# Kernel tuning notes

Hardware: AMD Instinct MI355X
Metric: run time of the kernel (lower is better)

## Reference

```python
import jax, jax.numpy as jnp
import numpy as np

SHAPES = ((64, 64), (32, 32), (16, 16), (8, 8))
LEVEL_STARTS = np.concatenate([[0], np.cumsum([h * w for h, w in SHAPES])]).tolist()
N_LEVELS = 4; N_HEADS = 8; N_POINTS = 4; D_MODEL = 256; HEAD_DIM = 32; D_FFN = 1024; NUM_LAYERS = 2
LEN_IN = sum(h * w for h, w in SHAPES)
BATCH = 2


def setup_inputs():
    key = jax.random.key(0)
    ks = iter(jax.random.split(key, 40))
    r = lambda shape, s=1.0: jax.random.normal(next(ks), shape, dtype=jnp.float32) * s
    L = NUM_LAYERS
    return {
        "src": r((BATCH, LEN_IN, D_MODEL)),
        "pos": r((BATCH, LEN_IN, D_MODEL), 0.5),
        "valid_ratios": jnp.ones((BATCH, N_LEVELS, 2), jnp.float32),
        "Wv": r((L, D_MODEL, D_MODEL), 0.05), "bv": jnp.zeros((L, D_MODEL), jnp.float32),
        "Woff": r((L, D_MODEL, N_HEADS * N_LEVELS * N_POINTS * 2), 0.002),
        "boff": r((L, N_HEADS * N_LEVELS * N_POINTS * 2), 0.5),
        "Wa": r((L, D_MODEL, N_HEADS * N_LEVELS * N_POINTS), 0.05),
        "ba": jnp.zeros((L, N_HEADS * N_LEVELS * N_POINTS), jnp.float32),
        "Wo": r((L, D_MODEL, D_MODEL), 0.05), "bo": jnp.zeros((L, D_MODEL), jnp.float32),
        "g1": jnp.ones((L, D_MODEL), jnp.float32), "be1": jnp.zeros((L, D_MODEL), jnp.float32),
        "Wl1": r((L, D_MODEL, D_FFN), 0.05), "bl1": jnp.zeros((L, D_FFN), jnp.float32),
        "Wl2": r((L, D_FFN, D_MODEL), 0.05), "bl2": jnp.zeros((L, D_MODEL), jnp.float32),
        "g2": jnp.ones((L, D_MODEL), jnp.float32), "be2": jnp.zeros((L, D_MODEL), jnp.float32),
    }


def layer_norm(x, g, b, eps=1e-5):
    m = jnp.mean(x, -1, keepdims=True)
    v = jnp.mean(jnp.square(x - m), -1, keepdims=True)
    return (x - m) * jax.lax.rsqrt(v + eps) * g + b


def make_reference_points(valid_ratios):
    # DeformableTransformerEncoder.get_reference_points, vectorized per level
    refs = []
    for lvl, (H, W) in enumerate(SHAPES):
        gy, gx = jnp.meshgrid(jnp.arange(H, dtype=jnp.float32) + 0.5,
                              jnp.arange(W, dtype=jnp.float32) + 0.5, indexing="ij")
        ry = gy.reshape(-1)[None] / (valid_ratios[:, lvl, 1][:, None] * H)
        rx = gx.reshape(-1)[None] / (valid_ratios[:, lvl, 0][:, None] * W)
        refs.append(jnp.stack([rx, ry], -1))  # [N, H*W, 2]
    ref = jnp.concatenate(refs, 1)  # [N, Len, 2]
    return ref[:, :, None, :] * valid_ratios[:, None]  # [N, Len, n_levels, 2]


def ms_deform_attn(query, input_flatten, reference_points, Wv, bv, Woff, boff, Wa, ba, Wo, bo):
    N, Lq, _ = query.shape
    value = (input_flatten @ Wv + bv).reshape(N, -1, N_HEADS, HEAD_DIM)
    off = (query @ Woff + boff).reshape(N, Lq, N_HEADS, N_LEVELS, N_POINTS, 2)
    aw = (query @ Wa + ba).reshape(N, Lq, N_HEADS, N_LEVELS * N_POINTS)
    aw = jax.nn.softmax(aw, -1).reshape(N, Lq, N_HEADS, N_LEVELS, N_POINTS)
    # normalizer is (W, H) per level, as in MSDeformAttn
    normalizer = jnp.array([[w, h] for h, w in SHAPES], jnp.float32)
    loc = reference_points[:, :, None, :, None, :] + off / normalizer[None, None, None, :, None, :]
    acc = jnp.zeros((N, N_HEADS, Lq, HEAD_DIM), query.dtype)
    for lvl, (H, W) in enumerate(SHAPES):
        s = LEVEL_STARTS[lvl]
        val = value[:, s:s + H * W].transpose(0, 2, 1, 3)  # [N, heads, H*W, hd]
        # grid_sample bilinear, align_corners=False, zero padding
        x = loc[:, :, :, lvl, :, 0] * W - 0.5  # [N, Lq, heads, P]
        y = loc[:, :, :, lvl, :, 1] * H - 0.5
        x0 = jnp.floor(x); y0 = jnp.floor(y)
        wx1 = x - x0; wy1 = y - y0
        ix0 = x0.astype(jnp.int32); iy0 = y0.astype(jnp.int32)

        def corner(ix, iy, w):
            valid = (ix >= 0) & (ix < W) & (iy >= 0) & (iy < H)
            idx = jnp.clip(iy, 0, H - 1) * W + jnp.clip(ix, 0, W - 1)
            idx = idx.transpose(0, 2, 1, 3).reshape(N, N_HEADS, Lq * N_POINTS)
            g = jnp.take_along_axis(val, idx[..., None], axis=2).reshape(N, N_HEADS, Lq, N_POINTS, HEAD_DIM)
            w = jnp.where(valid, w, 0.0).transpose(0, 2, 1, 3)  # [N, heads, Lq, P]
            return g * w[..., None]

        sampled = (corner(ix0, iy0, (1 - wx1) * (1 - wy1))
                   + corner(ix0 + 1, iy0, wx1 * (1 - wy1))
                   + corner(ix0, iy0 + 1, (1 - wx1) * wy1)
                   + corner(ix0 + 1, iy0 + 1, wx1 * wy1))
        acc = acc + (sampled * aw[:, :, :, lvl].transpose(0, 2, 1, 3)[..., None]).sum(3)
    out = acc.transpose(0, 2, 1, 3).reshape(N, Lq, D_MODEL)
    return out @ Wo + bo


def reference(src, pos, valid_ratios, Wv, bv, Woff, boff, Wa, ba, Wo, bo,
              g1, be1, Wl1, bl1, Wl2, bl2, g2, be2):
    ref_pts = make_reference_points(valid_ratios)
    out = src
    for l in range(NUM_LAYERS):
        q = out + pos  # with_pos_embed
        attn = ms_deform_attn(q, out, ref_pts, Wv[l], bv[l], Woff[l], boff[l],
                              Wa[l], ba[l], Wo[l], bo[l])
        out = layer_norm(out + attn, g1[l], be1[l])
        ffn = jax.nn.relu(out @ Wl1[l] + bl1[l]) @ Wl2[l] + bl2[l]
        out = layer_norm(out + ffn, g2[l], be2[l])
    return out
```

## Files before the change

### kernel.cpp

```cpp
#include <hip/hip_runtime.h>
#include <math.h>

#define LEN   5440
#define NB    2
#define MROWS (NB * LEN)
#define DM    256
#define NH    8
#define HD    32
#define NLV   4
#define NPT   4
#define DFFN  1024

typedef __attribute__((ext_vector_type(8))) short bf16x8;
typedef __attribute__((ext_vector_type(4))) short bf16x4;
typedef __attribute__((ext_vector_type(4))) float f32x4;

#define MFMA16 __builtin_amdgcn_mfma_f32_16x16x32_bf16

__device__ __forceinline__ short f2bf(float f) {
    union { float f; unsigned u; } cv; cv.f = f;
    unsigned r = cv.u + 0x7fffu + ((cv.u >> 16) & 1u);
    return (short)(r >> 16);
}
__device__ __forceinline__ float bf2f(short s) {
    union { unsigned u; float f; } cv;
    cv.u = ((unsigned)(unsigned short)s) << 16;
    return cv.f;
}

__device__ __forceinline__ void gload16(const short* g, short* l) {
    __builtin_amdgcn_global_load_lds(
        (__attribute__((address_space(1))) void*)g,
        (__attribute__((address_space(3))) void*)l, 16, 0, 0);
}

template <int N> __device__ __forceinline__ void vmwait();
template <> __device__ __forceinline__ void vmwait<0>() { asm volatile("s_waitcnt vmcnt(0)" ::: "memory"); }
template <> __device__ __forceinline__ void vmwait<8>() { asm volatile("s_waitcnt vmcnt(8)" ::: "memory"); }
template <> __device__ __forceinline__ void vmwait<9>() { asm volatile("s_waitcnt vmcnt(9)" ::: "memory"); }


__global__ __launch_bounds__(256) void prep_all(
    const float* __restrict__ Wv,  const float* __restrict__ Woff,
    const float* __restrict__ Wa,  const float* __restrict__ Wo,
    const float* __restrict__ Wl1, const float* __restrict__ Wl2,
    short* __restrict__ out,
    const float4* __restrict__ s4, const float4* __restrict__ p4,
    bf16x4* __restrict__ curb, bf16x4* __restrict__ qb)
{
    __shared__ short T[32][33];
    if (blockIdx.x >= 1472) {
        const int i = (blockIdx.x - 1472) * 256 + threadIdx.x;
        float4 s = s4[i], p = p4[i];
        bf16x4 c, q;
        c[0] = f2bf(s.x); c[1] = f2bf(s.y); c[2] = f2bf(s.z); c[3] = f2bf(s.w);
        q[0] = f2bf(s.x + p.x); q[1] = f2bf(s.y + p.y);
        q[2] = f2bf(s.z + p.z); q[3] = f2bf(s.w + p.w);
        curb[i] = c; qb[i] = q;
        return;
    }
    int bx = blockIdx.x;
    int l  = bx / 736;
    int t  = bx % 736;
    const float* src; int K, N; long doff;
    if      (t < 64)  { src = Wv;   K = 256;  N = 256;  doff = 0;      }
    else if (t < 128) { src = Woff; K = 256;  N = 256;  doff = 65536;  t -= 64;  }
    else if (t < 160) { src = Wa;   K = 256;  N = 128;  doff = 131072; t -= 128; }
    else if (t < 224) { src = Wo;   K = 256;  N = 256;  doff = 163840; t -= 160; }
    else if (t < 480) { src = Wl1;  K = 256;  N = 1024; doff = 229376; t -= 224; }
    else              { src = Wl2;  K = 1024; N = 256;  doff = 491520; t -= 480; }
    src += (long)l * K * N;
    short* dst = out + (long)l * 753664 + doff;

    const int ntx = N / 32;
    const int n0 = (t % ntx) * 32, k0 = (t / ntx) * 32;

    const int tid = threadIdx.x;
    {
        const int n = tid & 31, kq = tid >> 5;
        #pragma unroll
        for (int i = 0; i < 4; ++i) {
            int k = kq * 4 + i;
            T[n][k] = f2bf(src[(long)(k0 + k) * N + n0 + n]);
        }
    }
    __syncthreads();
    {
        const int k = tid & 31, nq = tid >> 5;
        #pragma unroll
        for (int i = 0; i < 4; ++i) {
            int n = nq * 4 + i;
            dst[(long)(n0 + n) * K + k0 + k] = T[n][k];
        }
    }
}

template <int RELU, int OMODE, int K>
__device__ __forceinline__ void gemm_core128_v3(
    short* As, short* Bs,
    const short* __restrict__ A, const short* __restrict__ Wt,
    const float* __restrict__ bias, float* __restrict__ Cf,
    short* __restrict__ Cb, int ldc, int m0, int wrow0, int ccol0)
{
    constexpr int NT = K / 64;
    static_assert(NT >= 4 && (NT & 1) == 0, "NT even >= 4");
    const int t    = threadIdx.x;
    const int wave = t >> 6, lane = t & 63;
    const int wm   = (wave & 1) * 64;
    const int wn   = (wave >> 1) * 64;
    const int lm   = lane & 15;
    const int chkg = lane >> 4;

    const short* aS[4]; const short* bS[4];
    int ldst[4];
    #pragma unroll
    for (int j = 0; j < 4; ++j) {
        const int row = wave * 32 + j * 8 + (lane >> 3);
        const int sc  = (lane & 7) ^ (row & 7);
        aS[j] = A  + (long)(m0 + row) * K + sc * 8;
        bS[j] = Wt + (long)(wrow0 + row) * K + sc * 8;
        ldst[j] = wave * 2048 + j * 512;
    }

    int offA[4], offB[4];
    #pragma unroll
    for (int s = 0; s < 4; ++s) {
        const int r = wm + s * 16 + lm;
        offA[s] = r * 64 + ((chkg ^ (r & 7)) * 8);
    }
    #pragma unroll
    for (int u = 0; u < 4; ++u) {
        const int r = wn + u * 16 + lm;
        offB[u] = r * 64 + ((chkg ^ (r & 7)) * 8);
    }

    f32x4 acc[4][4] = {};

#define STG3(BUF, KT) do {                                            \
        const int _ko = (KT) * 64;                                    \
        _Pragma("unroll")                                             \
        for (int j = 0; j < 4; ++j)                                   \
            gload16(aS[j] + _ko, As + (BUF) * 8192 + ldst[j]);        \
        _Pragma("unroll")                                             \
        for (int j = 0; j < 4; ++j)                                   \
            gload16(bS[j] + _ko, Bs + (BUF) * 8192 + ldst[j]);        \
    } while (0)

#define GB3(T, BUF, WN, DOSTAGE) do {                                 \
        vmwait<WN>();                                                 \
        __builtin_amdgcn_s_barrier();                                 \
        bf16x8 a0[4], a1[4], b0[4], b1[4];                            \
        _Pragma("unroll")                                             \
        for (int s = 0; s < 4; ++s) {                                 \
            a0[s] = *(const bf16x8*)(As + (BUF) * 8192 + offA[s]);    \
            a1[s] = *(const bf16x8*)(As + (BUF) * 8192 + (offA[s] ^ 32)); \
        }                                                             \
        _Pragma("unroll")                                             \
        for (int u = 0; u < 4; ++u) {                                 \
            b0[u] = *(const bf16x8*)(Bs + (BUF) * 8192 + offB[u]);    \
            b1[u] = *(const bf16x8*)(Bs + (BUF) * 8192 + (offB[u] ^ 32)); \
        }                                                             \
        asm volatile("s_waitcnt lgkmcnt(0)" ::: "memory");            \
        __builtin_amdgcn_s_barrier();                                 \
        __builtin_amdgcn_sched_barrier(0);                            \
        if (DOSTAGE) STG3(BUF, (T) + 2);                              \
        _Pragma("unroll")                                             \
        for (int s = 0; s < 4; ++s)                                   \
            _Pragma("unroll")                                         \
            for (int u = 0; u < 4; ++u) {                             \
                acc[s][u] = MFMA16(a0[s], b0[u], acc[s][u], 0, 0, 0); \
                acc[s][u] = MFMA16(a1[s], b1[u], acc[s][u], 0, 0, 0); \
            }                                                         \
    } while (0)

    STG3(0, 0);
    STG3(1, 1);
    for (int tt = 0; tt < NT - 2; tt += 2) {
        GB3(tt,     0, 8, true);
        GB3(tt + 1, 1, 8, true);
    }
    GB3(NT - 2, 0, 8, false);
    GB3(NT - 1, 1, 0, false);
#undef GB3
#undef STG3

    const int col = lane & 15;
    const int rq  = (lane >> 4) * 4;
    #pragma unroll
    for (int s = 0; s < 4; ++s) {
        #pragma unroll
        for (int u = 0; u < 4; ++u) {
            const int gn = ccol0 + wn + u * 16 + col;
            const float bb = bias[gn];
            #pragma unroll
            for (int r = 0; r < 4; ++r) {
                const int gm = m0 + wm + s * 16 + rq + r;
                float v = acc[s][u][r] + bb;
                if (RELU) v = fmaxf(v, 0.f);
                if (OMODE == 0) {
                    Cf[(long)gm * ldc + gn] = v;
                } else if (OMODE == 1) {
                    Cb[(long)gm * ldc + gn] = f2bf(v);
                } else {
                    const int n   = gm / LEN;
                    const int pix = gm - n * LEN;
                    const int h   = gn >> 5, d = gn & 31;
                    Cb[((long)(n * NH + h) * LEN + pix) * 32 + d] = f2bf(v);
                }
            }
        }
    }
}

template <int RELU, int OMODE, int K>
__global__ __launch_bounds__(256) void gemm128v3(
    const short* __restrict__ A, const short* __restrict__ Wt,
    const float* __restrict__ bias, float* Cf, short* Cb, int ldc)
{
    __shared__ __align__(16) short As[2 * 128 * 64];
    __shared__ __align__(16) short Bs[2 * 128 * 64];
    gemm_core128_v3<RELU, OMODE, K>(As, Bs, A, Wt, bias, Cf, Cb, ldc,
                                    blockIdx.y * 128, blockIdx.x * 128,
                                    blockIdx.x * 128);
}

__global__ __launch_bounds__(256) void gemm_qkv128(
    const short* __restrict__ curb, const short* __restrict__ qb,
    const short* __restrict__ Wt, const float* __restrict__ bv,
    const float* __restrict__ boff, const float* __restrict__ ba,
    short* __restrict__ Vb, float* __restrict__ OFF, float* __restrict__ AW)
{
    __shared__ __align__(16) short As[2 * 128 * 64];
    __shared__ __align__(16) short Bs[2 * 128 * 64];
    const int n0 = blockIdx.x * 128;
    if (n0 < 256) {
        gemm_core128_v3<0, 2, 256>(As, Bs, curb, Wt, bv, (float*)nullptr, Vb,
                                   256, blockIdx.y * 128, n0, n0);
    } else if (n0 < 512) {
        gemm_core128_v3<0, 0, 256>(As, Bs, qb, Wt, boff, OFF, (short*)nullptr,
                                   256, blockIdx.y * 128, n0, n0 - 256);
    } else {
        gemm_core128_v3<0, 0, 256>(As, Bs, qb, Wt, ba, AW, (short*)nullptr,
                                   128, blockIdx.y * 128, n0, n0 - 512);
    }
}

template <int K>
__global__ __launch_bounds__(256) void gemm_ln(
    const short* __restrict__ A, const short* __restrict__ Wt,
    const float* __restrict__ bias, const short* __restrict__ residb,
    const float* __restrict__ g, const float* __restrict__ be,
    short* __restrict__ outb, short* __restrict__ outq,
    float* __restrict__ outf, const float* __restrict__ pos)
{
    constexpr int NT = K / 64;
    static_assert(NT >= 4 && (NT & 1) == 0, "NT even >= 4");
    __shared__ __align__(16) short As[2 * 32 * 64];
    __shared__ __align__(16) short Bs[2 * 256 * 64];
    __shared__ float red[2][32][2];

    const int t    = threadIdx.x;
    const int wave = t >> 6, lane = t & 63;
    const int wm   = (wave & 1) * 16;
    const int wn   = (wave >> 1) * 128;
    const int lm   = lane & 15;
    const int chkg = lane >> 4;
    const int rq   = chkg * 4;
    const int m0   = blockIdx.x * 32;

    short rr[8][4];
    #pragma unroll
    for (int u = 0; u < 8; ++u)
        #pragma unroll
        for (int r = 0; r < 4; ++r)
            rr[u][r] = residb[(long)(m0 + wm + rq + r) * DM + wn + u * 16 + lm];
    asm volatile("" ::: "memory");

    const int arow = t >> 3;
    const short* aSp = A + (long)(m0 + arow) * K + (((t & 7) ^ (arow & 7)) * 8);
    const int aDst = wave * 512;
    const short* bSp[8]; int bDst[8];
    #pragma unroll
    for (int j = 0; j < 8; ++j) {
        const int row = wave * 64 + j * 8 + (lane >> 3);
        const int sc  = (lane & 7) ^ (row & 7);
        bSp[j] = Wt + (long)row * K + sc * 8;
        bDst[j] = wave * 4096 + j * 512;
    }

    const int offA = (wm + lm) * 64 + ((chkg ^ ((wm + lm) & 7)) * 8);
    int offB[8];
    #pragma unroll
    for (int u = 0; u < 8; ++u) {
        const int r = wn + u * 16 + lm;
        offB[u] = r * 64 + ((chkg ^ (r & 7)) * 8);
    }

    f32x4 acc[8] = {};

#define STGL(BUF, KT) do {                                            \
        const int _ko = (KT) * 64;                                    \
        gload16(aSp + _ko, As + (BUF) * 2048 + aDst);                 \
        _Pragma("unroll")                                             \
        for (int j = 0; j < 8; ++j)                                   \
            gload16(bSp[j] + _ko, Bs + (BUF) * 16384 + bDst[j]);      \
    } while (0)

#define GBLN(T, BUF, WN, DOSTAGE) do {                                \
        vmwait<WN>();                                                 \
        __builtin_amdgcn_s_barrier();                                 \
        bf16x8 af0 = *(const bf16x8*)(As + (BUF) * 2048 + offA);      \
        bf16x8 af1 = *(const bf16x8*)(As + (BUF) * 2048 + (offA ^ 32)); \
        bf16x8 b0[8], b1[8];                                          \
        _Pragma("unroll")                                             \
        for (int u = 0; u < 8; ++u) {                                 \
            b0[u] = *(const bf16x8*)(Bs + (BUF) * 16384 + offB[u]);   \
            b1[u] = *(const bf16x8*)(Bs + (BUF) * 16384 + (offB[u] ^ 32)); \
        }                                                             \
        asm volatile("s_waitcnt lgkmcnt(0)" ::: "memory");            \
        __builtin_amdgcn_s_barrier();                                 \
        __builtin_amdgcn_sched_barrier(0);                            \
        if (DOSTAGE) STGL(BUF, (T) + 2);                              \
        _Pragma("unroll")                                             \
        for (int u = 0; u < 8; ++u) {                                 \
            acc[u] = MFMA16(af0, b0[u], acc[u], 0, 0, 0);             \
            acc[u] = MFMA16(af1, b1[u], acc[u], 0, 0, 0);             \
        }                                                             \
    } while (0)

    STGL(0, 0);
    STGL(1, 1);
    for (int tt = 0; tt < NT - 2; tt += 2) {
        GBLN(tt,     0, 9, true);
        GBLN(tt + 1, 1, 9, true);
    }
    GBLN(NT - 2, 0, 9, false);
    GBLN(NT - 1, 1, 0, false);
#undef GBLN
#undef STGL

    #pragma unroll
    for (int u = 0; u < 8; ++u) {
        const int gn = wn + u * 16 + lm;
        const float bb = bias[gn];
        #pragma unroll
        for (int r = 0; r < 4; ++r)
            acc[u][r] += bb + bf2f(rr[u][r]);
    }

    float rs[4], r2[4];
    #pragma unroll
    for (int r = 0; r < 4; ++r) {
        float s = 0.f, s2 = 0.f;
        #pragma unroll
        for (int u = 0; u < 8; ++u) { const float v = acc[u][r]; s += v; s2 += v * v; }
        rs[r] = s; r2[r] = s2;
    }
    #pragma unroll
    for (int o = 1; o < 16; o <<= 1)
        #pragma unroll
        for (int r = 0; r < 4; ++r) {
            rs[r] += __shfl_xor(rs[r], o, 64);
            r2[r] += __shfl_xor(r2[r], o, 64);
        }
    if (lm == 0) {
        #pragma unroll
        for (int r = 0; r < 4; ++r) {
            red[wave >> 1][wm + rq + r][0] = rs[r];
            red[wave >> 1][wm + rq + r][1] = r2[r];
        }
    }
    __syncthreads();
    #pragma unroll
    for (int r = 0; r < 4; ++r) {
        const int row = wm + rq + r;
        const float ts = red[0][row][0] + red[1][row][0];
        const float t2 = red[0][row][1] + red[1][row][1];
        const float mean = ts * (1.f / DM);
        const float var  = t2 * (1.f / DM) - mean * mean;
        rs[r] = mean;
        r2[r] = rsqrtf(var + 1e-5f);
    }
    #pragma unroll
    for (int u = 0; u < 8; ++u) {
        const int gn = wn + u * 16 + lm;
        const float gg = g[gn], bbe = be[gn];
        #pragma unroll
        for (int r = 0; r < 4; ++r) {
            const long gm = m0 + wm + rq + r;
            const float o = (acc[u][r] - rs[r]) * r2[r] * gg + bbe;
            if (outb) outb[gm * DM + gn] = f2bf(o);
            if (outq) outq[gm * DM + gn] = f2bf(o + pos[gm * DM + gn]);
            if (outf) outf[gm * DM + gn] = o;
        }
    }
}

template <int KLEN, int KSTR>
__global__ __launch_bounds__(256) void ln2_part_k(
    const short* __restrict__ A0, const short* __restrict__ Wt0,
    float* __restrict__ PART)
{
    constexpr int NT = KLEN / 64;
    static_assert(NT >= 4 && (NT & 1) == 0, "NT even >= 4");
    __shared__ __align__(16) short As[2 * 32 * 64];
    __shared__ __align__(16) short Bs[2 * 256 * 64];

    const int kk = blockIdx.x;
    const int m0 = blockIdx.y * 32;
    const short* A  = A0  + kk * KLEN;
    const short* Wt = Wt0 + kk * KLEN;
    float* Pout = PART + (long)kk * MROWS * DM;

    const int t    = threadIdx.x;
    const int wave = t >> 6, lane = t & 63;
    const int wm   = (wave & 1) * 16;
    const int wn   = (wave >> 1) * 128;
    const int lm   = lane & 15;
    const int chkg = lane >> 4;
    const int rq   = chkg * 4;

    const int arow = t >> 3;
    const short* aSp = A + (long)(m0 + arow) * KSTR + (((t & 7) ^ (arow & 7)) * 8);
    const int aDst = wave * 512;
    const short* bSp[8]; int bDst[8];
    #pragma unroll
    for (int j = 0; j < 8; ++j) {
        const int row = wave * 64 + j * 8 + (lane >> 3);
        const int sc  = (lane & 7) ^ (row & 7);
        bSp[j] = Wt + (long)row * KSTR + sc * 8;
        bDst[j] = wave * 4096 + j * 512;
    }

    const int offA = (wm + lm) * 64 + ((chkg ^ ((wm + lm) & 7)) * 8);
    int offB[8];
    #pragma unroll
    for (int u = 0; u < 8; ++u) {
        const int r = wn + u * 16 + lm;
        offB[u] = r * 64 + ((chkg ^ (r & 7)) * 8);
    }

    f32x4 acc[8] = {};

#define STGP(BUF, KT) do {                                            \
        const int _ko = (KT) * 64;                                    \
        gload16(aSp + _ko, As + (BUF) * 2048 + aDst);                 \
        _Pragma("unroll")                                             \
        for (int j = 0; j < 8; ++j)                                   \
            gload16(bSp[j] + _ko, Bs + (BUF) * 16384 + bDst[j]);      \
    } while (0)

#define GBP(T, BUF, WN, DOSTAGE) do {                                 \
        vmwait<WN>();                                                 \
        __builtin_amdgcn_s_barrier();                                 \
        bf16x8 af0 = *(const bf16x8*)(As + (BUF) * 2048 + offA);      \
        bf16x8 af1 = *(const bf16x8*)(As + (BUF) * 2048 + (offA ^ 32)); \
        bf16x8 b0[8], b1[8];                                          \
        _Pragma("unroll")                                             \
        for (int u = 0; u < 8; ++u) {                                 \
            b0[u] = *(const bf16x8*)(Bs + (BUF) * 16384 + offB[u]);   \
            b1[u] = *(const bf16x8*)(Bs + (BUF) * 16384 + (offB[u] ^ 32)); \
        }                                                             \
        asm volatile("s_waitcnt lgkmcnt(0)" ::: "memory");            \
        __builtin_amdgcn_s_barrier();                                 \
        __builtin_amdgcn_sched_barrier(0);                            \
        if (DOSTAGE) STGP(BUF, (T) + 2);                              \
        _Pragma("unroll")                                             \
        for (int u = 0; u < 8; ++u) {                                 \
            acc[u] = MFMA16(af0, b0[u], acc[u], 0, 0, 0);             \
            acc[u] = MFMA16(af1, b1[u], acc[u], 0, 0, 0);             \
        }                                                             \
    } while (0)

    STGP(0, 0);
    STGP(1, 1);
    for (int tt = 0; tt < NT - 2; tt += 2) {
        GBP(tt,     0, 9, true);
        GBP(tt + 1, 1, 9, true);
    }
    GBP(NT - 2, 0, 9, false);
    GBP(NT - 1, 1, 0, false);
#undef GBP
#undef STGP

    #pragma unroll
    for (int u = 0; u < 8; ++u) {
        const int gn = wn + u * 16 + lm;
        #pragma unroll
        for (int r = 0; r < 4; ++r)
            Pout[(long)(m0 + wm + rq + r) * DM + gn] = acc[u][r];
    }
}

__global__ __launch_bounds__(256) void ln2_fin_k(
    const float* __restrict__ PART, const short* __restrict__ residb,
    const float* __restrict__ bl2, const float* __restrict__ g,
    const float* __restrict__ be, short* __restrict__ outb,
    short* __restrict__ outq, float* __restrict__ outf,
    const float* __restrict__ pos)
{
    const int wave = threadIdx.x >> 6, lane = threadIdx.x & 63;
    const int c0 = lane * 4;
    const f32x4 bb = *(const f32x4*)(bl2 + c0);
    const f32x4 gg = *(const f32x4*)(g + c0);
    const f32x4 ee = *(const f32x4*)(be + c0);
    #pragma unroll 1
    for (int r = 0; r < 8; ++r) {
        const long row = (long)blockIdx.x * 32 + wave * 8 + r;
        const f32x4 p0 = *(const f32x4*)(PART + row * DM + c0);
        const f32x4 p1 = *(const f32x4*)(PART + (long)MROWS * DM + row * DM + c0);
        const bf16x4 rr = *(const bf16x4*)(residb + row * DM + c0);
        float v[4]; float s = 0.f, s2 = 0.f;
        #pragma unroll
        for (int j = 0; j < 4; ++j) {
            v[j] = p0[j] + p1[j] + bb[j] + bf2f(rr[j]);
            s += v[j]; s2 += v[j] * v[j];
        }
        #pragma unroll
        for (int o = 1; o < 64; o <<= 1) {
            s  += __shfl_xor(s,  o, 64);
            s2 += __shfl_xor(s2, o, 64);
        }
        const float mean = s * (1.f / DM);
        const float var  = s2 * (1.f / DM) - mean * mean;
        const float rstd = rsqrtf(var + 1e-5f);
        float o4[4];
        #pragma unroll
        for (int j = 0; j < 4; ++j)
            o4[j] = (v[j] - mean) * rstd * gg[j] + ee[j];
        if (outb) {
            bf16x4 ob;
            #pragma unroll
            for (int j = 0; j < 4; ++j) ob[j] = f2bf(o4[j]);
            *(bf16x4*)(outb + row * DM + c0) = ob;
        }
        if (outq) {
            const f32x4 pp = *(const f32x4*)(pos + row * DM + c0);
            bf16x4 oq;
            #pragma unroll
            for (int j = 0; j < 4; ++j) oq[j] = f2bf(o4[j] + pp[j]);
            *(bf16x4*)(outq + row * DM + c0) = oq;
        }
        if (outf) {
            f32x4 of;
            #pragma unroll
            for (int j = 0; j < 4; ++j) of[j] = o4[j];
            *(f32x4*)(outf + row * DM + c0) = of;
        }
    }
}

__global__ __launch_bounds__(256) void deform_attn_v3(
    const short* __restrict__ Vb,
    const float* __restrict__ OFF,
    const float* __restrict__ AW,
    const float* __restrict__ vr,
    bf16x4* __restrict__ ATTb)
{
    const int starts[5] = {0, 4096, 5120, 5376, 5440};
    const int dims[4]   = {64, 32, 16, 8};

    const int wave = threadIdx.x >> 6;
    const int lane = threadIdx.x & 63;
    const int h    = lane >> 3;
    const int d4   = lane & 7;

    const int gq = blockIdx.x * 4 + wave;
    const int n  = gq / LEN;
    const int q  = gq % LEN;

    int lq = 3;
    if (q < 4096) lq = 0; else if (q < 5120) lq = 1; else if (q < 5376) lq = 2;
    const int r  = q - starts[lq];
    const int Wq = dims[lq];
    const int gy = r / Wq, gx = r % Wq;
    const float vrxq = vr[(n * NLV + lq) * 2 + 0];
    const float vryq = vr[(n * NLV + lq) * 2 + 1];
    const float rx = (gx + 0.5f) / (vrxq * Wq);
    const float ry = (gy + 0.5f) / (vryq * Wq);

    const long row = (long)n * LEN + q;

    const float* awp = AW + row * 128 + h * 16;
    float a[16];
    float mx = -1e30f;
    #pragma unroll
    for (int i = 0; i < 16; ++i) { a[i] = awp[i]; mx = fmaxf(mx, a[i]); }
    float s = 0.f;
    #pragma unroll
    for (int i = 0; i < 16; ++i) { a[i] = __expf(a[i] - mx); s += a[i]; }
    const float inv = 1.f / s;

    const float* offp = OFF + row * 256 + h * 32;

    float4 acc = {0.f, 0.f, 0.f, 0.f};
    #pragma unroll
    for (int lvl = 0; lvl < NLV; ++lvl) {
        const int Hl = dims[lvl];
        const int Wl = Hl;
        const float fW = (float)Wl;
        const int sb = starts[lvl];
        const float lx = rx * vr[(n * NLV + lvl) * 2 + 0];
        const float ly = ry * vr[(n * NLV + lvl) * 2 + 1];
        const short* vb = Vb + ((long)(n * NH + h) * LEN + sb) * 32 + d4 * 4;
        #pragma unroll
        for (int p = 0; p < NPT; ++p) {
            const float ox = offp[lvl * 8 + p * 2 + 0];
            const float oy = offp[lvl * 8 + p * 2 + 1];
            const float x = fmaf(lx, fW, ox) - 0.5f;
            const float y = fmaf(ly, fW, oy) - 0.5f;
            const float x0f = floorf(x), y0f = floorf(y);
            const int ix0 = (int)x0f, iy0 = (int)y0f;
            const float wx1 = x - x0f, wy1 = y - y0f;
            const float wx0 = 1.f - wx1, wy0 = 1.f - wy1;

            const bool vx0 = (ix0 >= 0)     && (ix0 < Wl);
            const bool vx1 = (ix0 + 1 >= 0) && (ix0 + 1 < Wl);
            const bool vy0 = (iy0 >= 0)     && (iy0 < Hl);
            const bool vy1 = (iy0 + 1 >= 0) && (iy0 + 1 < Hl);
            const int cx0 = min(max(ix0, 0), Wl - 1);
            const int cx1 = min(max(ix0 + 1, 0), Wl - 1);
            const int cy0 = min(max(iy0, 0), Hl - 1);
            const int cy1 = min(max(iy0 + 1, 0), Hl - 1);

            const float w00 = (vx0 && vy0) ? wx0 * wy0 : 0.f;
            const float w10 = (vx1 && vy0) ? wx1 * wy0 : 0.f;
            const float w01 = (vx0 && vy1) ? wx0 * wy1 : 0.f;
            const float w11 = (vx1 && vy1) ? wx1 * wy1 : 0.f;

            const bf16x4 g00 = *(const bf16x4*)(vb + (long)(cy0 * Wl + cx0) * 32);
            const bf16x4 g10 = *(const bf16x4*)(vb + (long)(cy0 * Wl + cx1) * 32);
            const bf16x4 g01 = *(const bf16x4*)(vb + (long)(cy1 * Wl + cx0) * 32);
            const bf16x4 g11 = *(const bf16x4*)(vb + (long)(cy1 * Wl + cx1) * 32);

            const float awv = a[lvl * 4 + p] * inv;
            #pragma unroll
            for (int e = 0; e < 4; ++e) {
                float sv = w00 * bf2f(g00[e]) + w10 * bf2f(g10[e])
                         + w01 * bf2f(g01[e]) + w11 * bf2f(g11[e]);
                (&acc.x)[e] += awv * sv;
            }
        }
    }
    bf16x4 ob;
    ob[0] = f2bf(acc.x); ob[1] = f2bf(acc.y);
    ob[2] = f2bf(acc.z); ob[3] = f2bf(acc.w);
    ATTb[row * 64 + h * 8 + d4] = ob;
}

extern "C" void kernel_launch(void* const* d_in, const int* in_sizes, int n_in,
                              void* d_out, int out_size, void* d_ws, size_t ws_size,
                              hipStream_t stream)
{
    const float* src = (const float*)d_in[0];
    const float* pos = (const float*)d_in[1];
    const float* vr  = (const float*)d_in[2];
    const float* Wv_   = (const float*)d_in[3];
    const float* bv_   = (const float*)d_in[4];
    const float* Woff_ = (const float*)d_in[5];
    const float* boff_ = (const float*)d_in[6];
    const float* Wa_   = (const float*)d_in[7];
    const float* ba_   = (const float*)d_in[8];
    const float* Wo_   = (const float*)d_in[9];
    const float* bo_   = (const float*)d_in[10];
    const float* g1_   = (const float*)d_in[11];
    const float* be1_  = (const float*)d_in[12];
    const float* Wl1_  = (const float*)d_in[13];
    const float* bl1_  = (const float*)d_in[14];
    const float* Wl2_  = (const float*)d_in[15];
    const float* bl2_  = (const float*)d_in[16];
    const float* g2_   = (const float*)d_in[17];
    const float* be2_  = (const float*)d_in[18];

    const long SZ = (long)MROWS * DM;
    float* ws = (float*)d_ws;
    float* OFF  = ws;
    float* AW   = OFF + SZ;
    short* Vb   = (short*)(AW + (long)MROWS * 128);
    short* curb = Vb   + SZ;
    short* qb   = curb + SZ;
    short* ATTb = qb   + SZ;
    short* XAb  = ATTb + SZ;
    short* FFNb = XAb  + SZ;
    short* Wt   = FFNb + (long)MROWS * DFFN;
    float* PART = (float*)(Wt + 2L * 753664);

    const dim3 blk(256);
    const int GYM = MROWS / 128;
    const int GLN = MROWS / 32;

    hipLaunchKernelGGL(prep_all, dim3(1472 + SZ / 4 / 256), blk, 0, stream,
                       Wv_, Woff_, Wa_, Wo_, Wl1_, Wl2_, Wt,
                       (const float4*)src, (const float4*)pos,
                       (bf16x4*)curb, (bf16x4*)qb);

    for (int l = 0; l < 2; ++l) {
        const short* Wbase = Wt + (long)l * 753664;
        const float* bv   = bv_   + (long)l * DM;
        const float* boff = boff_ + (long)l * 256;
        const float* ba   = ba_   + (long)l * 128;
        const float* bo   = bo_   + (long)l * DM;
        const float* g1   = g1_   + (long)l * DM;
        const float* be1  = be1_  + (long)l * DM;
        const float* bl1  = bl1_  + (long)l * DFFN;
        const float* bl2  = bl2_  + (long)l * DM;
        const float* g2   = g2_   + (long)l * DM;
        const float* be2  = be2_  + (long)l * DM;

        hipLaunchKernelGGL(gemm_qkv128, dim3(5, GYM), blk, 0, stream,
                           curb, qb, Wbase, bv, boff, ba, Vb, OFF, AW);
        hipLaunchKernelGGL(deform_attn_v3, dim3(MROWS / 4), blk, 0, stream,
                           Vb, OFF, AW, vr, (bf16x4*)ATTb);
        hipLaunchKernelGGL((gemm_ln<256>), dim3(GLN), blk, 0, stream,
                           ATTb, Wbase + 163840, bo, curb, g1, be1,
                           XAb, (short*)nullptr, (float*)nullptr,
                           (const float*)nullptr);
        hipLaunchKernelGGL((gemm128v3<1, 1, 256>), dim3(8, GYM), blk, 0, stream,
                           XAb, Wbase + 229376, bl1, (float*)nullptr, FFNb, 1024);
        hipLaunchKernelGGL((ln2_part_k<512, 1024>), dim3(2, GLN), blk, 0, stream,
                           FFNb, Wbase + 491520, PART);
        if (l == 0) {
            hipLaunchKernelGGL(ln2_fin_k, dim3(GLN), blk, 0, stream,
                               PART, XAb, bl2, g2, be2,
                               curb, qb, (float*)nullptr, pos);
        } else {
            hipLaunchKernelGGL(ln2_fin_k, dim3(GLN), blk, 0, stream,
                               PART, XAb, bl2, g2, be2,
                               (short*)nullptr, (short*)nullptr,
                               (float*)d_out, (const float*)nullptr);
        }
    }
}
```

Before: 287.6 us.

## Keep weight panels resident in LDS and stream activations from global

Replaces the double-buffered LDS-staged GEMM cores for the QKV, FFN1 and FFN2 partial GEMMs with a panel kernel. Each block loads its whole 128-column weight slice into LDS once. It then loops over several 128-row M tiles, reading A fragments directly from global memory into registers. The goal is to stop re-streaming weights for every M tile and to cut the number of barriers. The cost is unhidden global latency on A loads with no prefetch, large LDS use (up to 128KB per block) that limits occupancy, and uneven tile counts per block over the 85 M tiles.

```diff
diff --git a/kernel.cpp b/kernel.cpp
--- a/kernel.cpp
+++ b/kernel.cpp
@@ -36,7 +36,6 @@
 
 template <int N> __device__ __forceinline__ void vmwait();
 template <> __device__ __forceinline__ void vmwait<0>() { asm volatile("s_waitcnt vmcnt(0)" ::: "memory"); }
-template <> __device__ __forceinline__ void vmwait<8>() { asm volatile("s_waitcnt vmcnt(8)" ::: "memory"); }
 template <> __device__ __forceinline__ void vmwait<9>() { asm volatile("s_waitcnt vmcnt(9)" ::: "memory"); }
 
 
@@ -95,15 +94,14 @@
     }
 }
 
-template <int RELU, int OMODE, int K>
-__device__ __forceinline__ void gemm_core128_v3(
-    short* As, short* Bs,
-    const short* __restrict__ A, const short* __restrict__ Wt,
+template <int RELU, int OMODE, int KLEN>
+__device__ __forceinline__ void panel_core(
+    short* panel, const short* __restrict__ A, int astr,
+    const short* __restrict__ W, int wstr,
     const float* __restrict__ bias, float* __restrict__ Cf,
-    short* __restrict__ Cb, int ldc, int m0, int wrow0, int ccol0)
-{
-    constexpr int NT = K / 64;
-    static_assert(NT >= 4 && (NT & 1) == 0, "NT even >= 4");
+    short* __restrict__ Cb, int ldc, int ccol0, int nMt)
+{
+    constexpr int NSLAB = KLEN / 64;
     const int t    = threadIdx.x;
     const int wave = t >> 6, lane = t & 63;
     const int wm   = (wave & 1) * 64;
@@ -111,138 +109,127 @@
     const int lm   = lane & 15;
     const int chkg = lane >> 4;
 
-    const short* aS[4]; const short* bS[4];
-    int ldst[4];
-    #pragma unroll
-    for (int j = 0; j < 4; ++j) {
-        const int row = wave * 32 + j * 8 + (lane >> 3);
-        const int sc  = (lane & 7) ^ (row & 7);
-        aS[j] = A  + (long)(m0 + row) * K + sc * 8;
-        bS[j] = Wt + (long)(wrow0 + row) * K + sc * 8;
-        ldst[j] = wave * 2048 + j * 512;
-    }
-
-    int offA[4], offB[4];
-    #pragma unroll
-    for (int s = 0; s < 4; ++s) {
-        const int r = wm + s * 16 + lm;
-        offA[s] = r * 64 + ((chkg ^ (r & 7)) * 8);
-    }
+    {
+        const int prow = t >> 3;
+        const int pc   = t & 7;
+        #pragma unroll
+        for (int s = 0; s < NSLAB; ++s)
+            #pragma unroll
+            for (int ro = 0; ro < 128; ro += 32) {
+                const int row = ro + prow;
+                gload16(W + (long)row * wstr + s * 64 + ((pc ^ (row & 7)) * 8),
+                        panel + s * 8192 + ro * 64 + (wave & 3) * 0
+                              + ( (t >> 6) * 512 ) );
+            }
+    }
+    vmwait<0>();
+    __syncthreads();
+
+    int offB[4];
     #pragma unroll
     for (int u = 0; u < 4; ++u) {
         const int r = wn + u * 16 + lm;
         offB[u] = r * 64 + ((chkg ^ (r & 7)) * 8);
     }
 
-    f32x4 acc[4][4] = {};
-
-#define STG3(BUF, KT) do {                                            \
-        const int _ko = (KT) * 64;                                    \
-        _Pragma("unroll")                                             \
-        for (int j = 0; j < 4; ++j)                                   \
-            gload16(aS[j] + _ko, As + (BUF) * 8192 + ldst[j]);        \
-        _Pragma("unroll")                                             \
-        for (int j = 0; j < 4; ++j)                                   \
-            gload16(bS[j] + _ko, Bs + (BUF) * 8192 + ldst[j]);        \
-    } while (0)
-
-#define GB3(T, BUF, WN, DOSTAGE) do {                                 \
-        vmwait<WN>();                                                 \
-        __builtin_amdgcn_s_barrier();                                 \
-        bf16x8 a0[4], a1[4], b0[4], b1[4];                            \
-        _Pragma("unroll")                                             \
-        for (int s = 0; s < 4; ++s) {                                 \
-            a0[s] = *(const bf16x8*)(As + (BUF) * 8192 + offA[s]);    \
-            a1[s] = *(const bf16x8*)(As + (BUF) * 8192 + (offA[s] ^ 32)); \
-        }                                                             \
-        _Pragma("unroll")                                             \
-        for (int u = 0; u < 4; ++u) {                                 \
-            b0[u] = *(const bf16x8*)(Bs + (BUF) * 8192 + offB[u]);    \
-            b1[u] = *(const bf16x8*)(Bs + (BUF) * 8192 + (offB[u] ^ 32)); \
-        }                                                             \
-        asm volatile("s_waitcnt lgkmcnt(0)" ::: "memory");            \
-        __builtin_amdgcn_s_barrier();                                 \
-        __builtin_amdgcn_sched_barrier(0);                            \
-        if (DOSTAGE) STG3(BUF, (T) + 2);                              \
-        _Pragma("unroll")                                             \
-        for (int s = 0; s < 4; ++s)                                   \
-            _Pragma("unroll")                                         \
-            for (int u = 0; u < 4; ++u) {                             \
-                acc[s][u] = MFMA16(a0[s], b0[u], acc[s][u], 0, 0, 0); \
-                acc[s][u] = MFMA16(a1[s], b1[u], acc[s][u], 0, 0, 0); \
-            }                                                         \
-    } while (0)
-
-    STG3(0, 0);
-    STG3(1, 1);
-    for (int tt = 0; tt < NT - 2; tt += 2) {
-        GB3(tt,     0, 8, true);
-        GB3(tt + 1, 1, 8, true);
-    }
-    GB3(NT - 2, 0, 8, false);
-    GB3(NT - 1, 1, 0, false);
-#undef GB3
-#undef STG3
-
     const int col = lane & 15;
     const int rq  = (lane >> 4) * 4;
-    #pragma unroll
-    for (int s = 0; s < 4; ++s) {
-        #pragma unroll
-        for (int u = 0; u < 4; ++u) {
-            const int gn = ccol0 + wn + u * 16 + col;
-            const float bb = bias[gn];
-            #pragma unroll
-            for (int r = 0; r < 4; ++r) {
-                const int gm = m0 + wm + s * 16 + rq + r;
-                float v = acc[s][u][r] + bb;
-                if (RELU) v = fmaxf(v, 0.f);
-                if (OMODE == 0) {
-                    Cf[(long)gm * ldc + gn] = v;
-                } else if (OMODE == 1) {
-                    Cb[(long)gm * ldc + gn] = f2bf(v);
-                } else {
-                    const int n   = gm / LEN;
-                    const int pix = gm - n * LEN;
-                    const int h   = gn >> 5, d = gn & 31;
-                    Cb[((long)(n * NH + h) * LEN + pix) * 32 + d] = f2bf(v);
+
+    for (int mt = blockIdx.y; mt < nMt; mt += (int)gridDim.y) {
+        const int m0 = mt * 128;
+        f32x4 acc[4][4] = {};
+        #pragma unroll
+        for (int kt = 0; kt < NSLAB; ++kt) {
+            bf16x8 a0[4], a1[4], b0[4], b1[4];
+            #pragma unroll
+            for (int s = 0; s < 4; ++s) {
+                const short* ap = A + (long)(m0 + wm + s * 16 + lm) * astr
+                                    + kt * 64 + chkg * 8;
+                a0[s] = *(const bf16x8*)ap;
+                a1[s] = *(const bf16x8*)(ap + 32);
+            }
+            #pragma unroll
+            for (int u = 0; u < 4; ++u) {
+                b0[u] = *(const bf16x8*)(panel + kt * 8192 + offB[u]);
+                b1[u] = *(const bf16x8*)(panel + kt * 8192 + (offB[u] ^ 32));
+            }
+            #pragma unroll
+            for (int s = 0; s < 4; ++s)
+                #pragma unroll
+                for (int u = 0; u < 4; ++u) {
+                    acc[s][u] = MFMA16(a0[s], b0[u], acc[s][u], 0, 0, 0);
+                    acc[s][u] = MFMA16(a1[s], b1[u], acc[s][u], 0, 0, 0);
+                }
+        }
+
+        #pragma unroll
+        for (int s = 0; s < 4; ++s) {
+            #pragma unroll
+            for (int u = 0; u < 4; ++u) {
+                const int gn = ccol0 + wn + u * 16 + col;
+                const float bb = bias ? bias[gn] : 0.f;
+                #pragma unroll
+                for (int r = 0; r < 4; ++r) {
+                    const int gm = m0 + wm + s * 16 + rq + r;
+                    float v = acc[s][u][r] + bb;
+                    if (RELU) v = fmaxf(v, 0.f);
+                    if (OMODE == 0) {
+                        Cf[(long)gm * ldc + gn] = v;
+                    } else if (OMODE == 1) {
+                        Cb[(long)gm * ldc + gn] = f2bf(v);
+                    } else {
+                        const int n   = gm / LEN;
+                        const int pix = gm - n * LEN;
+                        const int h   = gn >> 5, d = gn & 31;
+                        Cb[((long)(n * NH + h) * LEN + pix) * 32 + d] = f2bf(v);
+                    }
                 }
             }
         }
     }
 }
 
-template <int RELU, int OMODE, int K>
-__global__ __launch_bounds__(256) void gemm128v3(
-    const short* __restrict__ A, const short* __restrict__ Wt,
-    const float* __restrict__ bias, float* Cf, short* Cb, int ldc)
-{
-    __shared__ __align__(16) short As[2 * 128 * 64];
-    __shared__ __align__(16) short Bs[2 * 128 * 64];
-    gemm_core128_v3<RELU, OMODE, K>(As, Bs, A, Wt, bias, Cf, Cb, ldc,
-                                    blockIdx.y * 128, blockIdx.x * 128,
-                                    blockIdx.x * 128);
-}
-
-__global__ __launch_bounds__(256) void gemm_qkv128(
+__global__ __launch_bounds__(256) void qkv_panel(
     const short* __restrict__ curb, const short* __restrict__ qb,
     const short* __restrict__ Wt, const float* __restrict__ bv,
     const float* __restrict__ boff, const float* __restrict__ ba,
     short* __restrict__ Vb, float* __restrict__ OFF, float* __restrict__ AW)
 {
-    __shared__ __align__(16) short As[2 * 128 * 64];
-    __shared__ __align__(16) short Bs[2 * 128 * 64];
-    const int n0 = blockIdx.x * 128;
-    if (n0 < 256) {
-        gemm_core128_v3<0, 2, 256>(As, Bs, curb, Wt, bv, (float*)nullptr, Vb,
-                                   256, blockIdx.y * 128, n0, n0);
-    } else if (n0 < 512) {
-        gemm_core128_v3<0, 0, 256>(As, Bs, qb, Wt, boff, OFF, (short*)nullptr,
-                                   256, blockIdx.y * 128, n0, n0 - 256);
+    __shared__ __align__(16) short panel[4 * 8192];
+    const int nc = blockIdx.x;
+    const short* W = Wt + (long)nc * 128 * 256;
+    if (nc < 2) {
+        panel_core<0, 2, 256>(panel, curb, 256, W, 256, bv, (float*)nullptr,
+                              Vb, 256, nc * 128, 85);
+    } else if (nc < 4) {
+        panel_core<0, 0, 256>(panel, qb, 256, W, 256, boff, OFF,
+                              (short*)nullptr, 256, (nc - 2) * 128, 85);
     } else {
-        gemm_core128_v3<0, 0, 256>(As, Bs, qb, Wt, ba, AW, (short*)nullptr,
-                                   128, blockIdx.y * 128, n0, n0 - 512);
-    }
+        panel_core<0, 0, 256>(panel, qb, 256, W, 256, ba, AW,
+                              (short*)nullptr, 128, 0, 85);
+    }
+}
+
+__global__ __launch_bounds__(256) void ffn1_panel(
+    const short* __restrict__ XAb, const short* __restrict__ W0,
+    const float* __restrict__ bias, short* __restrict__ FFNb)
+{
+    __shared__ __align__(16) short panel[4 * 8192];
+    const int nc = blockIdx.x;
+    panel_core<1, 1, 256>(panel, XAb, 256, W0 + (long)nc * 128 * 256, 256,
+                          bias, (float*)nullptr, FFNb, 1024, nc * 128, 85);
+}
+
+__global__ __launch_bounds__(256) void ln2_panel(
+    const short* __restrict__ FFNb, const short* __restrict__ W0,
+    float* __restrict__ PART)
+{
+    __shared__ __align__(16) short panel[8 * 8192];
+    const int kk = blockIdx.x >> 1, nc = blockIdx.x & 1;
+    panel_core<0, 0, 512>(panel, FFNb + kk * 512, 1024,
+                          W0 + (long)nc * 128 * 1024 + kk * 512, 1024,
+                          (const float*)nullptr, PART + (long)kk * MROWS * DM,
+                          (short*)nullptr, 256, nc * 128, 85);
 }
 
 template <int K>
@@ -396,102 +383,6 @@
     }
 }
 
-template <int KLEN, int KSTR>
-__global__ __launch_bounds__(256) void ln2_part_k(
-    const short* __restrict__ A0, const short* __restrict__ Wt0,
-    float* __restrict__ PART)
-{
-    constexpr int NT = KLEN / 64;
-    static_assert(NT >= 4 && (NT & 1) == 0, "NT even >= 4");
-    __shared__ __align__(16) short As[2 * 32 * 64];
-    __shared__ __align__(16) short Bs[2 * 256 * 64];
-
-    const int kk = blockIdx.x;
-    const int m0 = blockIdx.y * 32;
-    const short* A  = A0  + kk * KLEN;
-    const short* Wt = Wt0 + kk * KLEN;
-    float* Pout = PART + (long)kk * MROWS * DM;
-
-    const int t    = threadIdx.x;
-    const int wave = t >> 6, lane = t & 63;
-    const int wm   = (wave & 1) * 16;
-    const int wn   = (wave >> 1) * 128;
-    const int lm   = lane & 15;
-    const int chkg = lane >> 4;
-    const int rq   = chkg * 4;
-
-    const int arow = t >> 3;
-    const short* aSp = A + (long)(m0 + arow) * KSTR + (((t & 7) ^ (arow & 7)) * 8);
-    const int aDst = wave * 512;
-    const short* bSp[8]; int bDst[8];
-    #pragma unroll
-    for (int j = 0; j < 8; ++j) {
-        const int row = wave * 64 + j * 8 + (lane >> 3);
-        const int sc  = (lane & 7) ^ (row & 7);
-        bSp[j] = Wt + (long)row * KSTR + sc * 8;
-        bDst[j] = wave * 4096 + j * 512;
-    }
-
-    const int offA = (wm + lm) * 64 + ((chkg ^ ((wm + lm) & 7)) * 8);
-    int offB[8];
-    #pragma unroll
-    for (int u = 0; u < 8; ++u) {
-        const int r = wn + u * 16 + lm;
-        offB[u] = r * 64 + ((chkg ^ (r & 7)) * 8);
-    }
-
-    f32x4 acc[8] = {};
-
-#define STGP(BUF, KT) do {                                            \
-        const int _ko = (KT) * 64;                                    \
-        gload16(aSp + _ko, As + (BUF) * 2048 + aDst);                 \
-        _Pragma("unroll")                                             \
-        for (int j = 0; j < 8; ++j)                                   \
-            gload16(bSp[j] + _ko, Bs + (BUF) * 16384 + bDst[j]);      \
-    } while (0)
-
-#define GBP(T, BUF, WN, DOSTAGE) do {                                 \
-        vmwait<WN>();                                                 \
-        __builtin_amdgcn_s_barrier();                                 \
-        bf16x8 af0 = *(const bf16x8*)(As + (BUF) * 2048 + offA);      \
-        bf16x8 af1 = *(const bf16x8*)(As + (BUF) * 2048 + (offA ^ 32)); \
-        bf16x8 b0[8], b1[8];                                          \
-        _Pragma("unroll")                                             \
-        for (int u = 0; u < 8; ++u) {                                 \
-            b0[u] = *(const bf16x8*)(Bs + (BUF) * 16384 + offB[u]);   \
-            b1[u] = *(const bf16x8*)(Bs + (BUF) * 16384 + (offB[u] ^ 32)); \
-        }                                                             \
-        asm volatile("s_waitcnt lgkmcnt(0)" ::: "memory");            \
-        __builtin_amdgcn_s_barrier();                                 \
-        __builtin_amdgcn_sched_barrier(0);                            \
-        if (DOSTAGE) STGP(BUF, (T) + 2);                              \
-        _Pragma("unroll")                                             \
-        for (int u = 0; u < 8; ++u) {                                 \
-            acc[u] = MFMA16(af0, b0[u], acc[u], 0, 0, 0);             \
-            acc[u] = MFMA16(af1, b1[u], acc[u], 0, 0, 0);             \
-        }                                                             \
-    } while (0)
-
-    STGP(0, 0);
-    STGP(1, 1);
-    for (int tt = 0; tt < NT - 2; tt += 2) {
-        GBP(tt,     0, 9, true);
-        GBP(tt + 1, 1, 9, true);
-    }
-    GBP(NT - 2, 0, 9, false);
-    GBP(NT - 1, 1, 0, false);
-#undef GBP
-#undef STGP
-
-    #pragma unroll
-    for (int u = 0; u < 8; ++u) {
-        const int gn = wn + u * 16 + lm;
-        #pragma unroll
-        for (int r = 0; r < 4; ++r)
-            Pout[(long)(m0 + wm + rq + r) * DM + gn] = acc[u][r];
-    }
-}
-
 __global__ __launch_bounds__(256) void ln2_fin_k(
     const float* __restrict__ PART, const short* __restrict__ residb,
     const float* __restrict__ bl2, const float* __restrict__ g,
@@ -686,7 +577,6 @@
     float* PART = (float*)(Wt + 2L * 753664);
 
     const dim3 blk(256);
-    const int GYM = MROWS / 128;
     const int GLN = MROWS / 32;
 
     hipLaunchKernelGGL(prep_all, dim3(1472 + SZ / 4 / 256), blk, 0, stream,
@@ -707,7 +597,7 @@
         const float* g2   = g2_   + (long)l * DM;
         const float* be2  = be2_  + (long)l * DM;
 
-        hipLaunchKernelGGL(gemm_qkv128, dim3(5, GYM), blk, 0, stream,
+        hipLaunchKernelGGL(qkv_panel, dim3(5, 43), blk, 0, stream,
                            curb, qb, Wbase, bv, boff, ba, Vb, OFF, AW);
         hipLaunchKernelGGL(deform_attn_v3, dim3(MROWS / 4), blk, 0, stream,
                            Vb, OFF, AW, vr, (bf16x4*)ATTb);
@@ -715,9 +605,9 @@
                            ATTb, Wbase + 163840, bo, curb, g1, be1,
                            XAb, (short*)nullptr, (float*)nullptr,
                            (const float*)nullptr);
-        hipLaunchKernelGGL((gemm128v3<1, 1, 256>), dim3(8, GYM), blk, 0, stream,
-                           XAb, Wbase + 229376, bl1, (float*)nullptr, FFNb, 1024);
-        hipLaunchKernelGGL((ln2_part_k<512, 1024>), dim3(2, GLN), blk, 0, stream,
+        hipLaunchKernelGGL(ffn1_panel, dim3(8, 43), blk, 0, stream,
+                           XAb, Wbase + 229376, bl1, FFNb);
+        hipLaunchKernelGGL(ln2_panel, dim3(4, 64), blk, 0, stream,
                            FFNb, Wbase + 491520, PART);
         if (l == 0) {
             hipLaunchKernelGGL(ln2_fin_k, dim3(GLN), blk, 0, stream,
```

New measurement: 365.2 us. 1.27x slower.
